# Optimization experiments

Hardware: AMD Instinct MI355X
Metric: run time of the kernel (lower is better)

## Reference

```python
import jax, jax.numpy as jnp
import numpy as np


def setup_inputs() -> dict:
    key = jax.random.key(0)
    k1, k2, k3, k4 = jax.random.split(key, 4)
    B, H, S, D = 2, 16, 2048, 64
    q = jax.random.normal(k1, (B, H, S, D), dtype=jnp.float32)
    k = jax.random.normal(k2, (B, H, S, D), dtype=jnp.float32)
    v = jax.random.normal(k3, (B, H, S, D), dtype=jnp.float32)
    mask = jax.random.randint(k4, (1, 1, S, S), 0, 2, dtype=jnp.int32)
    return {"q": q, "k": k, "v": v, "mask": mask}


def reference(q, k, v, mask):
    # scores: [B,H,S,S] -- intentionally materialized as in the original
    d = k.shape[-1]
    scale = 1.0 / jnp.sqrt(jnp.asarray(d, dtype=q.dtype))
    x = jnp.einsum("bhqd,bhkd->bhqk", q, k) * scale
    x = x + mask.astype(x.dtype) * jnp.asarray(-10000.0, dtype=x.dtype)
    p = jax.nn.softmax(x, axis=-1)  # dropout is identity in eval mode
    return jnp.einsum("bhqk,bhkd->bhqd", p, v)
```

## Files before the change

kernel.cpp:

```cpp
#include <hip/hip_runtime.h>


#define S_LEN 2048
#define D_DIM 64
#define N_KT 32
#define NBH 32
#define TILE_SEGS 16
#define TILE_SHORTS 8192
#define SEG_U32 256

typedef __attribute__((ext_vector_type(8))) short bf16x8;
typedef __attribute__((ext_vector_type(16))) float f32x16;
typedef __attribute__((ext_vector_type(2))) __fp16 fp16x2;
typedef unsigned int u32;

#define C1 0.180336880111121f
#define CM (-14426.9504088896f)

static __device__ __forceinline__ unsigned short f2bf(float f) {
  union { float f; unsigned u; } x; x.f = f;
  return (unsigned short)((x.u + 0x8000u) >> 16);
}
static __device__ __forceinline__ unsigned packbf(float lo, float hi) {
  union { float f; unsigned u; } a, b; a.f = lo; b.f = hi;
  return ((a.u + 0x8000u) >> 16) | ((b.u + 0x8000u) & 0xffff0000u);
}
static __device__ __forceinline__ f32x16 zero16() {
  f32x16 z;
#pragma unroll
  for (int i = 0; i < 16; ++i) z[i] = 0.f;
  return z;
}
static __device__ __forceinline__ void dma16(const u32* g, u32* l) {
  __builtin_amdgcn_global_load_lds(
      (const __attribute__((address_space(1))) u32*)g,
      (__attribute__((address_space(3))) u32*)l, 16, 0, 0);
}
static __device__ __forceinline__ unsigned pkh(float lo, float hi) {
  union { fp16x2 h; unsigned u; } x;
  x.h = __builtin_amdgcn_cvt_pkrtz(lo, hi);
  return x.u;
}

__global__ __launch_bounds__(256) void prep_fused(
    const float* __restrict__ k, const float* __restrict__ v,
    const int* __restrict__ mask, unsigned short* __restrict__ kvws,
    u32* __restrict__ mw) {
  __shared__ unsigned short Kr[64 * 72];
  __shared__ unsigned short Vr[64 * 72];
  const int blk = blockIdx.x;
  const int t = threadIdx.x;
  if (blk < N_KT * NBH) {
    const int kt = blk & 31, bh = blk >> 5;
    const size_t goff = (size_t)bh * (S_LEN * D_DIM) + (size_t)kt * 64 * D_DIM;
    const float4* kg = (const float4*)(k + goff);
    const float4* vg = (const float4*)(v + goff);
#pragma unroll
    for (int j = 0; j < 4; ++j) {
      const int i = t + j * 256;
      const int row = i >> 4, c4 = i & 15;
      const float4 x = kg[i];
      ushort4 w;
      w.x = f2bf(x.x); w.y = f2bf(x.y); w.z = f2bf(x.z); w.w = f2bf(x.w);
      *(ushort4*)&Kr[row * 72 + c4 * 4] = w;
      const float4 y = vg[i];
      const unsigned p01 = pkh(y.x, y.y), p23 = pkh(y.z, y.w);
      uint2 vv; vv.x = p01; vv.y = p23;
      *(uint2*)&Vr[row * 72 + c4 * 4] = vv;
    }
    __syncthreads();
    uint4* img = (uint4*)(kvws + (size_t)(bh * N_KT + kt) * TILE_SHORTS);
    for (int c = t; c < 512; c += 256) {
      const int col = c & 31, hlc = (c >> 5) & 1, ks = (c >> 6) & 3, khc = c >> 8;
      img[c] = *(const uint4*)&Kr[(khc * 32 + col) * 72 + ks * 16 + hlc * 8];
    }
    for (int c = t; c < 512; c += 256) {
      const int col = c & 31, b = (c >> 5) & 1, hlc = (c >> 6) & 1, kcHi = c >> 7;
      const int d = b * 32 + col, kk = (2 * kcHi + hlc) * 8;
      union { unsigned short s[8]; uint4 u; } o;
#pragma unroll
      for (int jj = 0; jj < 8; ++jj) o.s[jj] = Vr[(kk + jj) * 72 + d];
      img[512 + c] = o.u;
    }
  } else {
    const int gt = (blk - N_KT * NBH) * 256 + t;
    const int q4 = gt & 3;
    const int kt = (gt >> 2) & 31;
    const int hl = (gt >> 7) & 1;
    const int row = gt >> 8;
    const int j0 = kt * 64 + 32 * (q4 >> 1) + 16 * (q4 & 1) + 4 * hl;
    const int* mr = mask + (size_t)row * S_LEN;
    const int4 a = *(const int4*)(mr + j0);
    const int4 b = *(const int4*)(mr + j0 + 8);
    uint4 w;
    w.x = (a.x == 0 ? 0x0000FFFFu : 0u) | (a.y == 0 ? 0xFFFF0000u : 0u);
    w.y = (a.z == 0 ? 0x0000FFFFu : 0u) | (a.w == 0 ? 0xFFFF0000u : 0u);
    w.z = (b.x == 0 ? 0x0000FFFFu : 0u) | (b.y == 0 ? 0xFFFF0000u : 0u);
    w.w = (b.z == 0 ? 0x0000FFFFu : 0u) | (b.w == 0 ? 0xFFFF0000u : 0u);
    *(uint4*)&mw[((size_t)(row * 2 + hl) * N_KT + kt) * 16 + q4 * 4] = w;
  }
}

__global__ __launch_bounds__(256, 4) void attn_fwd(
    const float* __restrict__ q, const unsigned short* __restrict__ kvws,
    const u32* __restrict__ mw, float* __restrict__ out) {
  const int lin = blockIdx.x + 32 * blockIdx.y;
  const int xcd = lin & 7;
  const int wk = lin >> 3;
  const int qt = wk & 31;
  const int bh = xcd * 4 + (wk >> 5);
  const size_t hoff = (size_t)bh * (S_LEN * D_DIM);

  __shared__ unsigned short sbuf[2][TILE_SHORTS];

  const int t = threadIdx.x;
  const int wave = t >> 6;
  const int lane = t & 63;
  const int col = lane & 31;
  const int hl = lane >> 5;
  const int qh = wave >> 1;
  const int kh = wave & 1;
  const int qg = qt * 64 + qh * 32 + col;

  bf16x8 bQ[4];
  {
    const float* qrow = q + hoff + (size_t)qg * D_DIM;
#pragma unroll
    for (int ks = 0; ks < 4; ++ks) {
      const float4 x0 = *(const float4*)(qrow + ks * 16 + hl * 8);
      const float4 x1 = *(const float4*)(qrow + ks * 16 + hl * 8 + 4);
      union { bf16x8 v; unsigned d[4]; } u;
      u.d[0] = packbf(x0.x * C1, x0.y * C1);
      u.d[1] = packbf(x0.z * C1, x0.w * C1);
      u.d[2] = packbf(x1.x * C1, x1.y * C1);
      u.d[3] = packbf(x1.z * C1, x1.w * C1);
      bQ[ks] = u.v;
    }
  }

  bf16x8 onesA;
  {
    union { bf16x8 v; unsigned d[4]; } u;
    u.d[0] = u.d[1] = u.d[2] = u.d[3] = 0x3C003C00u;
    onesA = u.v;
  }

  f32x16 oT0 = zero16(), oT1 = zero16(), oL = zero16();
  const uint4* mrow = (const uint4*)(mw + (size_t)(qg * 2 + hl) * N_KT * 16);
  const u32* img = (const u32*)(kvws + (size_t)bh * N_KT * TILE_SHORTS);
  const int seg0 = wave * 4;

  uint4 mq0, mq1;
  {
    const uint4* mp = mrow + kh * 2;
    asm volatile("global_load_dwordx4 %0, %2, off\n\t"
                 "global_load_dwordx4 %1, %3, off"
                 : "=&v"(mq0), "=&v"(mq1)
                 : "v"(mp), "v"(mp + 1)
                 : "memory");
  }
#pragma unroll
  for (int s = 0; s < 4; ++s)
    dma16(img + (size_t)(seg0 + s) * SEG_U32 + lane * 4,
          (u32*)&sbuf[0][0] + (seg0 + s) * SEG_U32);
#pragma unroll
  for (int s = 0; s < 4; ++s)
    dma16(img + (size_t)(TILE_SEGS + seg0 + s) * SEG_U32 + lane * 4,
          (u32*)&sbuf[1][0] + (seg0 + s) * SEG_U32);

  for (int kt = 0; kt < N_KT; ++kt) {
    const int p = kt & 1;
    if (kt < N_KT - 1) {
      asm volatile("s_waitcnt vmcnt(4)" ::: "memory");
    } else {
      asm volatile("s_waitcnt vmcnt(0)" ::: "memory");
    }
    __builtin_amdgcn_s_barrier();
    __builtin_amdgcn_sched_barrier(0);

    const unsigned short* Ksb = &sbuf[p][0];
    const unsigned short* Vtb = &sbuf[p][4096];
    const u32 mwv[8] = {mq0.x, mq0.y, mq0.z, mq0.w,
                        mq1.x, mq1.y, mq1.z, mq1.w};

    f32x16 sT = zero16();
    __builtin_amdgcn_s_setprio(1);
#pragma unroll
    for (int ks = 0; ks < 4; ++ks) {
      const bf16x8 aK =
          *(const bf16x8*)&Ksb[kh * 2048 + ks * 512 + hl * 256 + col * 8];
      sT = __builtin_amdgcn_mfma_f32_32x32x16_bf16(aK, bQ[ks], sT, 0, 0, 0);
    }
    __builtin_amdgcn_s_setprio(0);

    unsigned pw[8];
#pragma unroll
    for (int g2 = 0; g2 < 4; ++g2) {
      const float e0 = __builtin_amdgcn_exp2f(sT[g2 * 4 + 0]);
      const float e1 = __builtin_amdgcn_exp2f(sT[g2 * 4 + 1]);
      const float e2 = __builtin_amdgcn_exp2f(sT[g2 * 4 + 2]);
      const float e3 = __builtin_amdgcn_exp2f(sT[g2 * 4 + 3]);
      pw[g2 * 2 + 0] = pkh(e0, e1) & mwv[g2 * 2 + 0];
      pw[g2 * 2 + 1] = pkh(e2, e3) & mwv[g2 * 2 + 1];
    }

    __builtin_amdgcn_s_setprio(1);
#pragma unroll
    for (int ks2 = 0; ks2 < 2; ++ks2) {
      const unsigned d0 = pw[4 * ks2 + 0], d1 = pw[4 * ks2 + 1];
      const unsigned d2 = pw[4 * ks2 + 2], d3 = pw[4 * ks2 + 3];
      const unsigned s0 = hl ? d0 : d2;
      const unsigned s1 = hl ? d1 : d3;
      const unsigned r0 = (unsigned)__shfl_xor((int)s0, 32);
      const unsigned r1 = (unsigned)__shfl_xor((int)s1, 32);
      union { bf16x8 v; unsigned d[4]; } pf;
      pf.d[0] = hl ? r0 : d0;
      pf.d[1] = hl ? r1 : d1;
      pf.d[2] = hl ? d2 : r0;
      pf.d[3] = hl ? d3 : r1;
      const int kcHi = kh * 2 + ks2;
      const bf16x8 aV0 =
          *(const bf16x8*)&Vtb[kcHi * 1024 + hl * 512 + 0 * 256 + col * 8];
      const bf16x8 aV1 =
          *(const bf16x8*)&Vtb[kcHi * 1024 + hl * 512 + 1 * 256 + col * 8];
      oT0 = __builtin_amdgcn_mfma_f32_32x32x16_f16(aV0, pf.v, oT0, 0, 0, 0);
      oT1 = __builtin_amdgcn_mfma_f32_32x32x16_f16(aV1, pf.v, oT1, 0, 0, 0);
      oL = __builtin_amdgcn_mfma_f32_32x32x16_f16(onesA, pf.v, oL, 0, 0, 0);
    }
    __builtin_amdgcn_s_setprio(0);

    if (kt < N_KT - 1) {
      asm volatile("s_waitcnt lgkmcnt(0)" ::: "memory");
      __builtin_amdgcn_s_barrier();
      __builtin_amdgcn_sched_barrier(0);
      {
        const uint4* mp = mrow + (kt + 1) * 4 + kh * 2;
        asm volatile("global_load_dwordx4 %0, %2, off\n\t"
                     "global_load_dwordx4 %1, %3, off"
                     : "=&v"(mq0), "=&v"(mq1)
                     : "v"(mp), "v"(mp + 1)
                     : "memory");
      }
      if (kt < N_KT - 2) {
        const u32* g = img + (size_t)(kt + 2) * (TILE_SEGS * SEG_U32);
#pragma unroll
        for (int s = 0; s < 4; ++s)
          dma16(g + (size_t)(seg0 + s) * SEG_U32 + lane * 4,
                (u32*)&sbuf[p][0] + (seg0 + s) * SEG_U32);
      }
    }
  }

  __syncthreads();
  {
    float* xb = (float*)&sbuf[0][0];
    float* lb = (float*)((char*)&sbuf[0][0] + 17408);
    float* xr = xb + (size_t)(qh * 32 + col) * 68;
    if (kh) {
#pragma unroll
      for (int rg = 0; rg < 4; ++rg) {
        float4 w0, w1;
        w0.x = oT0[rg * 4 + 0]; w0.y = oT0[rg * 4 + 1];
        w0.z = oT0[rg * 4 + 2]; w0.w = oT0[rg * 4 + 3];
        w1.x = oT1[rg * 4 + 0]; w1.y = oT1[rg * 4 + 1];
        w1.z = oT1[rg * 4 + 2]; w1.w = oT1[rg * 4 + 3];
        *(float4*)(xr + 8 * rg + 4 * hl) = w0;
        *(float4*)(xr + 32 + 8 * rg + 4 * hl) = w1;
      }
      if (!hl) lb[qh * 32 + col] = oL[0];
    }
    __syncthreads();
    if (!kh) {
      const float inv = 1.0f / (oL[0] + lb[qh * 32 + col]);
      float* orow = out + hoff + (size_t)qg * D_DIM;
#pragma unroll
      for (int rg = 0; rg < 4; ++rg) {
        const float4 a0 = *(const float4*)(xr + 8 * rg + 4 * hl);
        const float4 a1 = *(const float4*)(xr + 32 + 8 * rg + 4 * hl);
        float4 w0, w1;
        w0.x = (oT0[rg * 4 + 0] + a0.x) * inv;
        w0.y = (oT0[rg * 4 + 1] + a0.y) * inv;
        w0.z = (oT0[rg * 4 + 2] + a0.z) * inv;
        w0.w = (oT0[rg * 4 + 3] + a0.w) * inv;
        w1.x = (oT1[rg * 4 + 0] + a1.x) * inv;
        w1.y = (oT1[rg * 4 + 1] + a1.y) * inv;
        w1.z = (oT1[rg * 4 + 2] + a1.z) * inv;
        w1.w = (oT1[rg * 4 + 3] + a1.w) * inv;
        *(float4*)(orow + 8 * rg + 4 * hl) = w0;
        *(float4*)(orow + 32 + 8 * rg + 4 * hl) = w1;
      }
    }
  }
}

#define LDK 72
#define LDV 72
__global__ __launch_bounds__(256, 2) void attn_fwd_self(
    const float* __restrict__ q, const float* __restrict__ k,
    const float* __restrict__ v, const int* __restrict__ mask,
    float* __restrict__ out) {
  const int qt = blockIdx.x;
  const int bh = blockIdx.y;
  const size_t hoff = (size_t)bh * (S_LEN * D_DIM);
  __shared__ unsigned short Ks[64 * LDK];
  __shared__ unsigned short Vt[64 * LDV];
  const int t = threadIdx.x;
  const int wave = t >> 6;
  const int lane = t & 63;
  const int col = lane & 31;
  const int hl = lane >> 5;
  const int sw = col >> 2;
  const int qg = qt * 128 + wave * 32 + col;
  bf16x8 bQ[4];
  {
    const float* qrow = q + hoff + (size_t)qg * D_DIM;
#pragma unroll
    for (int ks = 0; ks < 4; ++ks) {
      const float4 x0 = *(const float4*)(qrow + ks * 16 + hl * 8);
      const float4 x1 = *(const float4*)(qrow + ks * 16 + hl * 8 + 4);
      union { bf16x8 v; unsigned d[4]; } u;
      u.d[0] = packbf(x0.x, x0.y);
      u.d[1] = packbf(x0.z, x0.w);
      u.d[2] = packbf(x1.x, x1.y);
      u.d[3] = packbf(x1.z, x1.w);
      bQ[ks] = u.v;
    }
  }
  float4 pk[4], pv[4];
  {
    const float4* kg = (const float4*)(k + hoff);
    const float4* vg = (const float4*)(v + hoff);
#pragma unroll
    for (int j = 0; j < 4; ++j) { pk[j] = kg[t + j * 256]; pv[j] = vg[t + j * 256]; }
  }
  f32x16 oT0 = zero16(), oT1 = zero16();
  float lacc = 0.f;
  const int* mrow = mask + (size_t)qg * S_LEN;
  for (int kt = 0; kt < N_KT; ++kt) {
    __syncthreads();
#pragma unroll
    for (int j = 0; j < 4; ++j) {
      const int i = t + j * 256;
      const int row = i >> 4, c4 = i & 15;
      ushort4 w;
      w.x = f2bf(pk[j].x); w.y = f2bf(pk[j].y);
      w.z = f2bf(pk[j].z); w.w = f2bf(pk[j].w);
      *(ushort4*)&Ks[row * LDK + c4 * 4] = w;
      const int swc = 8 * (((row >> 3) + c4) & 7) + (row & 7);
      Vt[(4 * c4 + 0) * LDV + swc] = f2bf(pv[j].x);
      Vt[(4 * c4 + 1) * LDV + swc] = f2bf(pv[j].y);
      Vt[(4 * c4 + 2) * LDV + swc] = f2bf(pv[j].z);
      Vt[(4 * c4 + 3) * LDV + swc] = f2bf(pv[j].w);
    }
    __syncthreads();
    if (kt + 1 < N_KT) {
      const float4* kg = (const float4*)(k + hoff + (size_t)(kt + 1) * 64 * D_DIM);
      const float4* vg = (const float4*)(v + hoff + (size_t)(kt + 1) * 64 * D_DIM);
#pragma unroll
      for (int j = 0; j < 4; ++j) { pk[j] = kg[t + j * 256]; pv[j] = vg[t + j * 256]; }
    }
    int4 mq[2][4];
#pragma unroll
    for (int kb = 0; kb < 2; ++kb)
#pragma unroll
      for (int g = 0; g < 4; ++g)
        mq[kb][g] = *(const int4*)(mrow + kt * 64 + kb * 32 + g * 8 + hl * 4);
    f32x16 sT0 = zero16(), sT1 = zero16();
#pragma unroll
    for (int ks = 0; ks < 4; ++ks) {
      const bf16x8 aK0 = *(const bf16x8*)&Ks[col * LDK + ks * 16 + hl * 8];
      const bf16x8 aK1 = *(const bf16x8*)&Ks[(32 + col) * LDK + ks * 16 + hl * 8];
      sT0 = __builtin_amdgcn_mfma_f32_32x32x16_bf16(aK0, bQ[ks], sT0, 0, 0, 0);
      sT1 = __builtin_amdgcn_mfma_f32_32x32x16_bf16(aK1, bQ[ks], sT1, 0, 0, 0);
    }
    unsigned pw[2][8];
#pragma unroll
    for (int kb = 0; kb < 2; ++kb) {
      const f32x16 sT = kb ? sT1 : sT0;
      float e[16];
#pragma unroll
      for (int g = 0; g < 4; ++g) {
        const int4 mv = mq[kb][g];
        const int* mvp = &mv.x;
#pragma unroll
        for (int r3 = 0; r3 < 4; ++r3) {
          const int reg = g * 4 + r3;
          const float bias = mvp[r3] ? CM : 0.0f;
          const float ev = __builtin_amdgcn_exp2f(fmaf(sT[reg], C1, bias));
          e[reg] = ev;
          lacc += ev;
        }
        pw[kb][g * 2 + 0] = packbf(e[g * 4 + 0], e[g * 4 + 1]);
        pw[kb][g * 2 + 1] = packbf(e[g * 4 + 2], e[g * 4 + 3]);
      }
    }
#pragma unroll
    for (int ks = 0; ks < 4; ++ks) {
      const int kb = ks >> 1, h = ks & 1;
      const unsigned d0 = pw[kb][4 * h + 0], d1 = pw[kb][4 * h + 1];
      const unsigned d2 = pw[kb][4 * h + 2], d3 = pw[kb][4 * h + 3];
      const unsigned s0 = hl ? d0 : d2;
      const unsigned s1 = hl ? d1 : d3;
      const unsigned r0 = (unsigned)__shfl_xor((int)s0, 32);
      const unsigned r1 = (unsigned)__shfl_xor((int)s1, 32);
      union { bf16x8 v; unsigned d[4]; } pf;
      pf.d[0] = hl ? r0 : d0;
      pf.d[1] = hl ? r1 : d1;
      pf.d[2] = hl ? d2 : r0;
      pf.d[3] = hl ? d3 : r1;
      const int cpr = 8 * (((2 * ks + hl) + sw) & 7);
      const bf16x8 aV0 = *(const bf16x8*)&Vt[col * LDV + cpr];
      const bf16x8 aV1 = *(const bf16x8*)&Vt[(32 + col) * LDV + cpr];
      oT0 = __builtin_amdgcn_mfma_f32_32x32x16_bf16(aV0, pf.v, oT0, 0, 0, 0);
      oT1 = __builtin_amdgcn_mfma_f32_32x32x16_bf16(aV1, pf.v, oT1, 0, 0, 0);
    }
  }
  const float ltot = lacc + __shfl_xor(lacc, 32);
  const float inv = 1.0f / ltot;
  float* orow = out + hoff + (size_t)qg * D_DIM;
#pragma unroll
  for (int rg = 0; rg < 4; ++rg) {
    float4 w0, w1;
    w0.x = oT0[rg * 4 + 0] * inv; w0.y = oT0[rg * 4 + 1] * inv;
    w0.z = oT0[rg * 4 + 2] * inv; w0.w = oT0[rg * 4 + 3] * inv;
    w1.x = oT1[rg * 4 + 0] * inv; w1.y = oT1[rg * 4 + 1] * inv;
    w1.z = oT1[rg * 4 + 2] * inv; w1.w = oT1[rg * 4 + 3] * inv;
    *(float4*)(orow + 8 * rg + 4 * hl) = w0;
    *(float4*)(orow + 32 + 8 * rg + 4 * hl) = w1;
  }
}

extern "C" void kernel_launch(void* const* d_in, const int* in_sizes, int n_in,
                              void* d_out, int out_size, void* d_ws, size_t ws_size,
                              hipStream_t stream) {
  const float* q = (const float*)d_in[0];
  const float* k = (const float*)d_in[1];
  const float* v = (const float*)d_in[2];
  const int* mask = (const int*)d_in[3];
  float* out = (float*)d_out;

  const size_t kv_shorts = (size_t)NBH * N_KT * TILE_SHORTS;
  const size_t mw_words = (size_t)S_LEN * 2 * N_KT * 16;
  const size_t need = kv_shorts * sizeof(unsigned short) + mw_words * 4;

  if (ws_size >= need) {
    unsigned short* kvws = (unsigned short*)d_ws;
    u32* mwp = (u32*)(kvws + kv_shorts);
    prep_fused<<<dim3(N_KT * NBH + (S_LEN * 2 * N_KT * 4) / 256), dim3(256), 0,
                 stream>>>(k, v, mask, kvws, mwp);
    attn_fwd<<<dim3(S_LEN / 64, NBH), dim3(256), 0, stream>>>(q, kvws, mwp, out);
  } else {
    attn_fwd_self<<<dim3(S_LEN / 128, NBH), dim3(256), 0, stream>>>(q, k, v, mask, out);
  }
}
```

Measured before the change: 167.0 us.

## Process two K/V tiles per barrier with a four-buffer LDS pipeline

```diff
diff --git a/kernel.cpp b/kernel.cpp
--- a/kernel.cpp
+++ b/kernel.cpp
@@ -101,7 +101,7 @@
   }
 }
 
-__global__ __launch_bounds__(256, 4) void attn_fwd(
+__global__ __launch_bounds__(256, 2) void attn_fwd(
     const float* __restrict__ q, const unsigned short* __restrict__ kvws,
     const u32* __restrict__ mw, float* __restrict__ out) {
   const int lin = blockIdx.x + 32 * blockIdx.y;
@@ -111,7 +111,7 @@
   const int bh = xcd * 4 + (wk >> 5);
   const size_t hoff = (size_t)bh * (S_LEN * D_DIM);
 
-  __shared__ unsigned short sbuf[2][TILE_SHORTS];
+  __shared__ unsigned short sbuf[4][TILE_SHORTS];
 
   const int t = threadIdx.x;
   const int wave = t >> 6;
@@ -150,39 +150,9 @@
   const u32* img = (const u32*)(kvws + (size_t)bh * N_KT * TILE_SHORTS);
   const int seg0 = wave * 4;
 
-  uint4 mq0, mq1;
-  {
-    const uint4* mp = mrow + kh * 2;
-    asm volatile("global_load_dwordx4 %0, %2, off\n\t"
-                 "global_load_dwordx4 %1, %3, off"
-                 : "=&v"(mq0), "=&v"(mq1)
-                 : "v"(mp), "v"(mp + 1)
-                 : "memory");
-  }
-#pragma unroll
-  for (int s = 0; s < 4; ++s)
-    dma16(img + (size_t)(seg0 + s) * SEG_U32 + lane * 4,
-          (u32*)&sbuf[0][0] + (seg0 + s) * SEG_U32);
-#pragma unroll
-  for (int s = 0; s < 4; ++s)
-    dma16(img + (size_t)(TILE_SEGS + seg0 + s) * SEG_U32 + lane * 4,
-          (u32*)&sbuf[1][0] + (seg0 + s) * SEG_U32);
-
-  for (int kt = 0; kt < N_KT; ++kt) {
-    const int p = kt & 1;
-    if (kt < N_KT - 1) {
-      asm volatile("s_waitcnt vmcnt(4)" ::: "memory");
-    } else {
-      asm volatile("s_waitcnt vmcnt(0)" ::: "memory");
-    }
-    __builtin_amdgcn_s_barrier();
-    __builtin_amdgcn_sched_barrier(0);
-
-    const unsigned short* Ksb = &sbuf[p][0];
-    const unsigned short* Vtb = &sbuf[p][4096];
-    const u32 mwv[8] = {mq0.x, mq0.y, mq0.z, mq0.w,
-                        mq1.x, mq1.y, mq1.z, mq1.w};
-
+  auto tile_body = [&](const unsigned short* base, const u32* mwv) {
+    const unsigned short* Ksb = base;
+    const unsigned short* Vtb = base + 4096;
     f32x16 sT = zero16();
     __builtin_amdgcn_s_setprio(1);
 #pragma unroll
@@ -192,7 +162,6 @@
       sT = __builtin_amdgcn_mfma_f32_32x32x16_bf16(aK, bQ[ks], sT, 0, 0, 0);
     }
     __builtin_amdgcn_s_setprio(0);
-
     unsigned pw[8];
 #pragma unroll
     for (int g2 = 0; g2 < 4; ++g2) {
@@ -203,7 +172,6 @@
       pw[g2 * 2 + 0] = pkh(e0, e1) & mwv[g2 * 2 + 0];
       pw[g2 * 2 + 1] = pkh(e2, e3) & mwv[g2 * 2 + 1];
     }
-
     __builtin_amdgcn_s_setprio(1);
 #pragma unroll
     for (int ks2 = 0; ks2 < 2; ++ks2) {
@@ -228,25 +196,75 @@
       oL = __builtin_amdgcn_mfma_f32_32x32x16_f16(onesA, pf.v, oL, 0, 0, 0);
     }
     __builtin_amdgcn_s_setprio(0);
-
-    if (kt < N_KT - 1) {
+  };
+
+  uint4 mqA0, mqA1, mqB0, mqB1;
+  {
+    const uint4* mpA = mrow + 0 * 4 + kh * 2;
+    const uint4* mpB = mrow + 1 * 4 + kh * 2;
+    asm volatile("global_load_dwordx4 %0, %4, off\n\t"
+                 "global_load_dwordx4 %1, %5, off\n\t"
+                 "global_load_dwordx4 %2, %6, off\n\t"
+                 "global_load_dwordx4 %3, %7, off"
+                 : "=&v"(mqA0), "=&v"(mqA1), "=&v"(mqB0), "=&v"(mqB1)
+                 : "v"(mpA), "v"(mpA + 1), "v"(mpB), "v"(mpB + 1)
+                 : "memory");
+  }
+#pragma unroll
+  for (int tb = 0; tb < 4; ++tb)
+#pragma unroll
+    for (int s = 0; s < 4; ++s)
+      dma16(img + (size_t)tb * (TILE_SEGS * SEG_U32) +
+                (size_t)(seg0 + s) * SEG_U32 + lane * 4,
+            (u32*)&sbuf[tb][0] + (seg0 + s) * SEG_U32);
+
+  for (int it = 0; it < N_KT / 2; ++it) {
+    const int pA = (it & 1) * 2;
+    const int pB = pA + 1;
+    if (it < N_KT / 2 - 1) {
+      asm volatile("s_waitcnt vmcnt(8)" ::: "memory");
+    } else {
+      asm volatile("s_waitcnt vmcnt(0)" ::: "memory");
+    }
+    __builtin_amdgcn_s_barrier();
+    __builtin_amdgcn_sched_barrier(0);
+
+    const u32 mwvA[8] = {mqA0.x, mqA0.y, mqA0.z, mqA0.w,
+                         mqA1.x, mqA1.y, mqA1.z, mqA1.w};
+    const u32 mwvB[8] = {mqB0.x, mqB0.y, mqB0.z, mqB0.w,
+                         mqB1.x, mqB1.y, mqB1.z, mqB1.w};
+
+    tile_body(&sbuf[pA][0], mwvA);
+    tile_body(&sbuf[pB][0], mwvB);
+
+    if (it < N_KT / 2 - 1) {
       asm volatile("s_waitcnt lgkmcnt(0)" ::: "memory");
       __builtin_amdgcn_s_barrier();
       __builtin_amdgcn_sched_barrier(0);
       {
-        const uint4* mp = mrow + (kt + 1) * 4 + kh * 2;
-        asm volatile("global_load_dwordx4 %0, %2, off\n\t"
-                     "global_load_dwordx4 %1, %3, off"
-                     : "=&v"(mq0), "=&v"(mq1)
-                     : "v"(mp), "v"(mp + 1)
+        const int tA = 2 * it + 2, tB = 2 * it + 3;
+        const uint4* mpA = mrow + tA * 4 + kh * 2;
+        const uint4* mpB = mrow + tB * 4 + kh * 2;
+        asm volatile("global_load_dwordx4 %0, %4, off\n\t"
+                     "global_load_dwordx4 %1, %5, off\n\t"
+                     "global_load_dwordx4 %2, %6, off\n\t"
+                     "global_load_dwordx4 %3, %7, off"
+                     : "=&v"(mqA0), "=&v"(mqA1), "=&v"(mqB0), "=&v"(mqB1)
+                     : "v"(mpA), "v"(mpA + 1), "v"(mpB), "v"(mpB + 1)
                      : "memory");
       }
-      if (kt < N_KT - 2) {
-        const u32* g = img + (size_t)(kt + 2) * (TILE_SEGS * SEG_U32);
+      if (it < N_KT / 2 - 2) {
+        const int tA = 2 * it + 4, tB = 2 * it + 5;
+        const u32* gA = img + (size_t)tA * (TILE_SEGS * SEG_U32);
+        const u32* gB = img + (size_t)tB * (TILE_SEGS * SEG_U32);
 #pragma unroll
         for (int s = 0; s < 4; ++s)
-          dma16(g + (size_t)(seg0 + s) * SEG_U32 + lane * 4,
-                (u32*)&sbuf[p][0] + (seg0 + s) * SEG_U32);
+          dma16(gA + (size_t)(seg0 + s) * SEG_U32 + lane * 4,
+                (u32*)&sbuf[pA][0] + (seg0 + s) * SEG_U32);
+#pragma unroll
+        for (int s = 0; s < 4; ++s)
+          dma16(gB + (size_t)(seg0 + s) * SEG_U32 + lane * 4,
+                (u32*)&sbuf[pB][0] + (seg0 + s) * SEG_U32);
       }
     }
   }
```

After: 167.1 us. About the same (+0.1%).
